# Optimization experiments

Hardware: AMD Instinct MI355X
Metric: run time of the kernel (lower is better)

Reference implementation:

```python
import jax, jax.numpy as jnp
import numpy as np

B, S, H = 1, 2048, 2048
NH = 16            # num attention heads
QLR = 1536         # q_lora_rank
KVLR = 512         # kv_lora_rank
DR = 64            # qk_rope_head_dim
DN = 128           # qk_nope_head_dim
DV = 128           # v_head_dim
DQK = DN + DR      # qk_head_dim = 192
EPS = 1e-6


def rmsnorm(x, w):
    xf = x.astype(jnp.float32)
    var = jnp.mean(xf * xf, axis=-1, keepdims=True)
    return (xf * jax.lax.rsqrt(var + EPS)).astype(x.dtype) * w


def rotate_half(x):
    d = x.shape[-1] // 2
    return jnp.concatenate([-x[..., d:], x[..., :d]], axis=-1)


def rope_interleave(x, cos, sin):
    # x: [b, h, s, d]; de-interleave pairs (even dims -> first half, odd -> second)
    b, h, s, d = x.shape
    x = x.reshape(b, h, s, d // 2, 2).swapaxes(-1, -2).reshape(b, h, s, d)
    return x * cos + rotate_half(x) * sin


def setup_inputs() -> dict:
    key = jax.random.key(0)
    ks = jax.random.split(key, 8)
    std = 0.02
    hidden_states = jax.random.normal(ks[0], (B, S, H), jnp.float32)
    # real rotary cos/sin for a 64-dim rope slice
    pos = jnp.arange(S, dtype=jnp.float32)
    inv_freq = 1.0 / (10000.0 ** (jnp.arange(0, DR, 2, dtype=jnp.float32) / DR))
    ang = pos[:, None] * inv_freq[None, :]            # [S, DR//2]
    emb = jnp.concatenate([ang, ang], axis=-1)        # [S, DR]
    cos = jnp.broadcast_to(jnp.cos(emb)[None], (B, S, DR)).astype(jnp.float32)
    sin = jnp.broadcast_to(jnp.sin(emb)[None], (B, S, DR)).astype(jnp.float32)
    # weights stored [in, out]
    wq_a = jax.random.normal(ks[1], (H, QLR), jnp.float32) * std
    q_ln = jnp.ones((QLR,), jnp.float32)
    wq_b = jax.random.normal(ks[2], (QLR, NH * DQK), jnp.float32) * std
    wkv_a = jax.random.normal(ks[3], (H, KVLR + DR), jnp.float32) * std
    kv_ln = jnp.ones((KVLR,), jnp.float32)
    wkv_b = jax.random.normal(ks[4], (KVLR, NH * (DN + DV)), jnp.float32) * std
    wo = jax.random.normal(ks[5], (NH * DV, H), jnp.float32) * std
    return {"hidden_states": hidden_states, "cos": cos, "sin": sin,
            "wq_a": wq_a, "q_ln": q_ln, "wq_b": wq_b,
            "wkv_a": wkv_a, "kv_ln": kv_ln, "wkv_b": wkv_b, "wo": wo}


def reference(hidden_states, cos, sin, wq_a, q_ln, wq_b, wkv_a, kv_ln, wkv_b, wo):
    b, s, _ = hidden_states.shape
    # low-rank Q: a-proj -> RMSNorm -> b-proj
    q = rmsnorm(hidden_states @ wq_a, q_ln) @ wq_b           # [b, s, NH*DQK]
    q = q.reshape(b, s, NH, DQK).transpose(0, 2, 1, 3)       # [b, NH, s, DQK]
    q_pass, q_rot = q[..., :DN], q[..., DN:]
    # compressed KV with shared rope key
    ckv = hidden_states @ wkv_a                               # [b, s, KVLR+DR]
    kv_c, k_rot = ckv[..., :KVLR], ckv[..., KVLR:]
    kv = (rmsnorm(kv_c, kv_ln) @ wkv_b).reshape(b, s, NH, DN + DV).transpose(0, 2, 1, 3)
    k_pass, v = kv[..., :DN], kv[..., DN:]
    k_rot = k_rot[:, None, :, :]                              # [b, 1, s, DR]
    cos4, sin4 = cos[:, None], sin[:, None]
    q_rot = rope_interleave(q_rot, cos4, sin4)
    k_rot = rope_interleave(k_rot, cos4, sin4)
    k_rot = jnp.broadcast_to(k_rot, (b, NH, s, DR))
    qs = jnp.concatenate([q_pass, q_rot], axis=-1)            # [b, NH, s, DQK]
    ks_ = jnp.concatenate([k_pass, k_rot], axis=-1)
    scaling = DQK ** -0.5
    scores = jnp.einsum('bhqd,bhkd->bhqk', qs, ks_) * scaling
    causal = jnp.tril(jnp.ones((s, s), bool))
    scores = jnp.where(causal, scores, jnp.finfo(scores.dtype).min)
    probs = jax.nn.softmax(scores.astype(jnp.float32), axis=-1).astype(qs.dtype)
    out = jnp.einsum('bhqk,bhkd->bhqd', probs, v)             # [b, NH, s, DV]
    out = out.transpose(0, 2, 1, 3).reshape(b, s, NH * DV)
    return out @ wo
```

## Files before the change

kernel.cpp:

```cpp
#include <hip/hip_runtime.h>
#include <hip/hip_bf16.h>
#include <stdint.h>

#define S_    2048
#define H_    2048
#define NH_   16
#define QLR_  1536
#define KVLR_ 512
#define DR_   64
#define DN_   128
#define DV_   128
#define DQK_  192
#define QW_   (NH_*DQK_)
#define KVW_  (NH_*(DN_+DV_))
#define CKVW_ (KVLR_+DR_)

typedef __attribute__((ext_vector_type(8))) short short8;
typedef __attribute__((ext_vector_type(4))) float floatx4;

__device__ __forceinline__ unsigned short f2bf(float f) {
    unsigned u = __float_as_uint(f);
    unsigned r = u + 0x7fffu + ((u >> 16) & 1u);
    return (unsigned short)(r >> 16);
}
__device__ __forceinline__ float bf2f(unsigned short h) {
    return __uint_as_float(((unsigned)h) << 16);
}
__device__ __forceinline__ void store_out(float* p, float v) { *p = v; }
__device__ __forceinline__ void store_out(unsigned short* p, float v) { *p = f2bf(v); }

typedef const __attribute__((address_space(1))) unsigned int* gas_ptr;
typedef __attribute__((address_space(3))) unsigned int* las_ptr;
__device__ __forceinline__ void gload16(const void* g, void* l) {
    __builtin_amdgcn_global_load_lds((gas_ptr)g, (las_ptr)l, 16, 0, 0);
}

__device__ __forceinline__ int xcd_swz(int orig, int nwg) {
    int q8 = nwg >> 3, r8 = nwg & 7;
    int xcd = orig & 7, jj = orig >> 3;
    return (xcd < r8 ? xcd * (q8 + 1) : r8 * (q8 + 1) + (xcd - r8) * q8) + jj;
}

#define GEMM_STAGE(b, k0) do {                                               \
        _Pragma("unroll")                                                    \
        for (int sub = 0; sub < 2; ++sub) {                                  \
            int m = tid >> 2, k8 = tid & 3;                                  \
            gload16(A + (size_t)(bm + m) * lda + (k0) + sub * 32 + k8 * 8,   \
                    &As[b][sub][tid * 8]);                                   \
        }                                                                    \
        _Pragma("unroll")                                                    \
        for (int sub = 0; sub < 2; ++sub)                                    \
            _Pragma("unroll")                                                \
            for (int j = 0; j < BN / 64; ++j) {                              \
                int ch = j * 256 + tid;                                      \
                int n = ch >> 2, k8 = ch & 3;                                \
                int nrow = bn + n; if (nrow >= N) nrow = N - 1;              \
                gload16(Bt + (size_t)nrow * K + (k0) + sub * 32 + k8 * 8,    \
                        &Bs[b][sub][ch * 8]);                                \
            }                                                                \
    } while (0)

#define GEMM_COMPUTE_SUB(sub) do {                                           \
        short8 a[2], b[NFR];                                                 \
        _Pragma("unroll")                                                    \
        for (int mi = 0; mi < 2; ++mi)                                       \
            a[mi] = *(const short8*)&As[cur][sub][(wm + mi * 16 + cc) * 32 + g * 8]; \
        _Pragma("unroll")                                                    \
        for (int ni = 0; ni < NFR; ++ni)                                     \
            b[ni] = *(const short8*)&Bs[cur][sub][(wn + ni * 16 + cc) * 32 + g * 8]; \
        __builtin_amdgcn_s_setprio(1);                                       \
        _Pragma("unroll")                                                    \
        for (int mi = 0; mi < 2; ++mi)                                       \
            _Pragma("unroll")                                                \
            for (int ni = 0; ni < NFR; ++ni)                                 \
                acc[mi][ni] = __builtin_amdgcn_mfma_f32_16x16x32_bf16(       \
                    a[mi], b[ni], acc[mi][ni], 0, 0, 0);                     \
        __builtin_amdgcn_s_setprio(0);                                       \
    } while (0)

template <typename OutT, int BN>
__global__ __launch_bounds__(256) void gemm_bf16_db(
    const unsigned short* __restrict__ A, const unsigned short* __restrict__ Bt,
    OutT* __restrict__ C, int M, int N, int K, int lda, int ldc)
{
    constexpr int NFR = BN / 32;
    __shared__ unsigned short As[2][2][64 * 32];
    __shared__ unsigned short Bs[2][2][BN * 32];

    const int tid = threadIdx.x;
    const int l = tid & 63;
    const int g = l >> 4, cc = l & 15;
    const int w = tid >> 6;
    const int wm = (w >> 1) * 32, wn = (w & 1) * (BN / 2);

    const int nwg = gridDim.x * gridDim.y;
    const int wg = xcd_swz(blockIdx.y * gridDim.x + blockIdx.x, nwg);
    const int bm = (wg / gridDim.x) * 64;
    const int bn = (wg % gridDim.x) * BN;

    floatx4 acc[2][NFR];
#pragma unroll
    for (int i = 0; i < 2; i++)
#pragma unroll
        for (int j = 0; j < NFR; j++) acc[i][j] = (floatx4){0.f, 0.f, 0.f, 0.f};

    GEMM_STAGE(0, 0);
    __syncthreads();
    int cur = 0;

    for (int k0 = 0; k0 < K; k0 += 64) {
        if (k0 + 64 < K) GEMM_STAGE(cur ^ 1, k0 + 64);
        GEMM_COMPUTE_SUB(0);
        GEMM_COMPUTE_SUB(1);
        __syncthreads();
        cur ^= 1;
    }

#pragma unroll
    for (int mi = 0; mi < 2; ++mi)
#pragma unroll
        for (int ni = 0; ni < NFR; ++ni)
#pragma unroll
            for (int i = 0; i < 4; ++i) {
                int row = bm + wm + mi * 16 + g * 4 + i;
                int col = bn + wn + ni * 16 + cc;
                if (col < N) store_out(&C[(size_t)row * ldc + col], acc[mi][ni][i]);
            }
}

__global__ __launch_bounds__(256) void gemm_bf16_dual(
    const unsigned short* __restrict__ A, const unsigned short* __restrict__ Bt,
    float* __restrict__ C0, float* __restrict__ C1,
    int M, int N, int K, int lda, int ldc0, int ldc1)
{
    constexpr int BN = 128;
    constexpr int NFR = 4;
    __shared__ unsigned short As[2][2][64 * 32];
    __shared__ unsigned short Bs[2][2][BN * 32];

    const int tid = threadIdx.x;
    const int l = tid & 63;
    const int g = l >> 4, cc = l & 15;
    const int w = tid >> 6;
    const int wm = (w >> 1) * 32, wn = (w & 1) * (BN / 2);

    const int nwg = gridDim.x * gridDim.y;
    const int wg = xcd_swz(blockIdx.y * gridDim.x + blockIdx.x, nwg);
    const int bm = (wg / gridDim.x) * 64;
    const int bn = (wg % gridDim.x) * BN;

    floatx4 acc[2][NFR];
#pragma unroll
    for (int i = 0; i < 2; i++)
#pragma unroll
        for (int j = 0; j < NFR; j++) acc[i][j] = (floatx4){0.f, 0.f, 0.f, 0.f};

    GEMM_STAGE(0, 0);
    __syncthreads();
    int cur = 0;

    for (int k0 = 0; k0 < K; k0 += 64) {
        if (k0 + 64 < K) GEMM_STAGE(cur ^ 1, k0 + 64);
        GEMM_COMPUTE_SUB(0);
        GEMM_COMPUTE_SUB(1);
        __syncthreads();
        cur ^= 1;
    }

#pragma unroll
    for (int mi = 0; mi < 2; ++mi)
#pragma unroll
        for (int ni = 0; ni < NFR; ++ni)
#pragma unroll
            for (int i = 0; i < 4; ++i) {
                int row = bm + wm + mi * 16 + g * 4 + i;
                int col = bn + wn + ni * 16 + cc;
                if (col < QLR_)
                    C0[(size_t)row * ldc0 + col] = acc[mi][ni][i];
                else if (col < N)
                    C1[(size_t)row * ldc1 + (col - QLR_)] = acc[mi][ni][i];
            }
}

__global__ __launch_bounds__(256) void cast_bf16(
    const float* __restrict__ in, unsigned short* __restrict__ out, int n)
{
    int i = (blockIdx.x * 256 + threadIdx.x) * 4;
    if (i >= n) return;
    float4 v = *(const float4*)&in[i];
    ushort4 u;
    u.x = f2bf(v.x); u.y = f2bf(v.y); u.z = f2bf(v.z); u.w = f2bf(v.w);
    *(ushort4*)&out[i] = u;
}

__global__ __launch_bounds__(256) void transpose_cast(
    const float* __restrict__ W, unsigned short* __restrict__ Wt, int K, int N,
    float scl)
{
    __shared__ float t[32][33];
    const int n0 = blockIdx.x * 32, k0 = blockIdx.y * 32;
    const int tx = threadIdx.x & 31, ty4 = (threadIdx.x >> 5) * 4;
#pragma unroll
    for (int j = 0; j < 4; ++j)
        t[ty4 + j][tx] = W[(size_t)(k0 + ty4 + j) * N + n0 + tx];
    __syncthreads();
#pragma unroll
    for (int j = 0; j < 4; ++j)
        Wt[(size_t)(n0 + ty4 + j) * K + k0 + tx] = f2bf(t[tx][ty4 + j] * scl);
}

__global__ __launch_bounds__(256) void rmsnorm_bf16out(
    const float* __restrict__ x, const float* __restrict__ w,
    unsigned short* __restrict__ y, int cols, int xstride)
{
    const float* xr = x + (size_t)blockIdx.x * xstride;
    unsigned short* yr = y + (size_t)blockIdx.x * cols;
    const int tid = threadIdx.x;
    float ss = 0.f;
    for (int c = tid; c < cols; c += 256) { float v = xr[c]; ss += v * v; }
#pragma unroll
    for (int off = 32; off > 0; off >>= 1) ss += __shfl_xor(ss, off);
    __shared__ float red[4];
    if ((tid & 63) == 0) red[tid >> 6] = ss;
    __syncthreads();
    ss = red[0] + red[1] + red[2] + red[3];
    const float inv = rsqrtf(ss / (float)cols + 1e-6f);
    for (int c = tid; c < cols; c += 256) yr[c] = f2bf(xr[c] * inv * w[c]);
}

__global__ void rope_q_bf(unsigned short* __restrict__ q,
                          const float* __restrict__ cs, const float* __restrict__ sn)
{
    int t = blockIdx.x * 256 + threadIdx.x;
    int chunk = t >> 5, j = t & 31;
    int s = chunk >> 4, h = chunk & 15;
    unsigned short* x = q + (size_t)s * QW_ + h * DQK_ + DN_;
    float e = bf2f(x[2 * j]), o = bf2f(x[2 * j + 1]);
    float c = cs[s * DR_ + j], si = sn[s * DR_ + j];
    unsigned short u = f2bf(e * c - o * si);
    unsigned short v = f2bf(o * c + e * si);
    x[j] = u; x[j + 32] = v;
}

__global__ __launch_bounds__(256) void prep_k(
    const unsigned short* __restrict__ kvb, const float* __restrict__ ckv,
    const float* __restrict__ cs, const float* __restrict__ sn,
    unsigned short* __restrict__ kg)
{
    const int s = blockIdx.x, tid = threadIdx.x;
    __shared__ unsigned short rot[64];
    if (tid < 32) {
        int j = tid;
        const float* x = ckv + (size_t)s * CKVW_ + KVLR_;
        float e = x[2 * j], o = x[2 * j + 1];
        float c = cs[s * DR_ + j], si = sn[s * DR_ + j];
        rot[j] = f2bf(e * c - o * si);
        rot[j + 32] = f2bf(o * c + e * si);
    }
    __syncthreads();
    const int sw = s & 7;
    for (int ch = tid; ch < 384; ch += 256) {
        int hh = ch / 24, d8 = ch % 24;
        short8 v;
        if (d8 < 16)
            v = *(const short8*)&kvb[(size_t)s * KVW_ + hh * 256 + d8 * 8];
        else
            v = *(const short8*)&rot[(d8 - 16) * 8];
        int d8s = d8 ^ sw;
        *(short8*)&kg[((size_t)hh * S_ + s) * 192 + d8s * 8] = v;
    }
}

__global__ __launch_bounds__(256) void transpose_v(
    const unsigned short* __restrict__ kvb, unsigned short* __restrict__ vt)
{
    __shared__ unsigned short t[32][36];
    const int dv0 = blockIdx.x * 32, s0 = blockIdx.y * 32, h = blockIdx.z;
    const int r = threadIdx.x >> 3, c4 = threadIdx.x & 7;
    ushort4 ld = *(const ushort4*)&kvb[(size_t)(s0 + r) * KVW_ + h * 256 + 128 + dv0 + c4 * 4];
    t[r][c4 * 4 + 0] = ld.x; t[r][c4 * 4 + 1] = ld.y;
    t[r][c4 * 4 + 2] = ld.z; t[r][c4 * 4 + 3] = ld.w;
    __syncthreads();
    ushort4 st;
    st.x = t[c4 * 4 + 0][r]; st.y = t[c4 * 4 + 1][r];
    st.z = t[c4 * 4 + 2][r]; st.w = t[c4 * 4 + 3][r];
    *(ushort4*)&vt[(size_t)(h * 128 + dv0 + r) * S_ + s0 + c4 * 4] = st;
}

__global__ __launch_bounds__(256, 3) void flash_attn7(
    const unsigned short* __restrict__ qg, const unsigned short* __restrict__ kg,
    const unsigned short* __restrict__ vt,
    unsigned short* __restrict__ op0, unsigned short* __restrict__ op1,
    float* __restrict__ mlp)
{
    const int bid = blockIdx.x;
    const int qblk = 31 - (bid >> 5);
    const int low5 = bid & 31;
    const int h = low5 & 15;
    const int sp = low5 >> 4;
    const int pb = h * 32 + qblk;

    __shared__ unsigned short sm[2 * 6144 + 2 * 4096 + 4 * 640];
    unsigned short* Kb = sm;
    unsigned short* Vb = sm + 12288;
    const int tid = threadIdx.x;
    const int w = tid >> 6;
    const int l = tid & 63, g = l >> 4, cc = l & 15;
    unsigned short* Pw = sm + 20480 + w * 640;

    const int qmin = qblk * 64 + w * 16;
    const int q_lane = qmin + cc;
    const int wave_qmax = qmin + 15;
    const int HT = qblk + 1;
    const int kt_begin = sp * HT, kt_end = kt_begin + HT;

    const unsigned short* kh = kg + (size_t)h * S_ * 192;
    const unsigned short* vh = vt + (size_t)(h * 128) * S_;

    short8 qf[6];
    {
        const unsigned short* qb = qg + (size_t)q_lane * QW_ + h * DQK_;
#pragma unroll
        for (int k6 = 0; k6 < 6; ++k6)
            qf[k6] = *(const short8*)&qb[k6 * 32 + g * 8];
    }

    floatx4 accO[8];
#pragma unroll
    for (int nt = 0; nt < 8; ++nt) accO[nt] = (floatx4){0.f, 0.f, 0.f, 0.f};
    float m_r = -1e30f, l_r = 0.f;

#define STAGE_KV(b, kt) do {                                             \
        const unsigned short* ksrc = kh + (size_t)(kt) * 32 * 192;       \
        _Pragma("unroll")                                                \
        for (int j = 0; j < 3; ++j) {                                    \
            int ch = j * 256 + tid;                                      \
            gload16(ksrc + ch * 8, Kb + (b) * 6144 + ch * 8);            \
        }                                                                \
        const int krow = (kt) * 32;                                      \
        _Pragma("unroll")                                                \
        for (int j = 0; j < 2; ++j) {                                    \
            int ch = j * 256 + tid;                                      \
            int dv = ch >> 2, j8 = ch & 3;                               \
            gload16(vh + (size_t)dv * S_ + krow + j8 * 8,                \
                    Vb + (b) * 4096 + ch * 8);                           \
        }                                                                \
    } while (0)

    STAGE_KV(0, kt_begin);
    int cur = 0;

    for (int kt = kt_begin; kt < kt_end; ++kt) {
        const int krow0 = kt * 32;
        __syncthreads();
        if (kt + 1 < kt_end) STAGE_KV(cur ^ 1, kt + 1);

        if (krow0 <= wave_qmax) {
            const unsigned short* Kc = Kb + cur * 6144;
            const unsigned short* Vc = Vb + cur * 4096;
            const int swz = (cc & 7) << 3;

            floatx4 s0 = (floatx4){0.f, 0.f, 0.f, 0.f};
            floatx4 s1 = (floatx4){0.f, 0.f, 0.f, 0.f};
            __builtin_amdgcn_s_setprio(1);
#pragma unroll
            for (int k6 = 0; k6 < 6; ++k6) {
                short8 b0 = *(const short8*)&Kc[cc * 192 + ((k6 * 32 + g * 8) ^ swz)];
                short8 b1 = *(const short8*)&Kc[(16 + cc) * 192 + ((k6 * 32 + g * 8) ^ swz)];
                s0 = __builtin_amdgcn_mfma_f32_16x16x32_bf16(b0, qf[k6], s0, 0, 0, 0);
                s1 = __builtin_amdgcn_mfma_f32_16x16x32_bf16(b1, qf[k6], s1, 0, 0, 0);
            }
            __builtin_amdgcn_s_setprio(0);

            float v0[4], v1[4];
            if (krow0 + 31 <= qmin) {
#pragma unroll
                for (int i = 0; i < 4; ++i) { v0[i] = s0[i]; v1[i] = s1[i]; }
            } else {
#pragma unroll
                for (int i = 0; i < 4; ++i) {
                    v0[i] = (krow0 + g * 4 + i) <= q_lane ? s0[i] : -1e30f;
                    v1[i] = (krow0 + 16 + g * 4 + i) <= q_lane ? s1[i] : -1e30f;
                }
            }
            float mt = fmaxf(fmaxf(fmaxf(v0[0], v0[1]), fmaxf(v0[2], v0[3])),
                             fmaxf(fmaxf(v1[0], v1[1]), fmaxf(v1[2], v1[3])));
            mt = fmaxf(mt, __shfl_xor(mt, 16));
            mt = fmaxf(mt, __shfl_xor(mt, 32));

            if (!__all(mt <= m_r + 6.0f)) {
                float mn = fmaxf(m_r, mt);
                float alpha = exp2f(m_r - mn);
                m_r = mn;
                l_r *= alpha;
                float aB[4];
#pragma unroll
                for (int i = 0; i < 4; ++i) aB[i] = __shfl(alpha, g * 4 + i);
#pragma unroll
                for (int nt = 0; nt < 8; ++nt)
#pragma unroll
                    for (int i = 0; i < 4; ++i) accO[nt][i] *= aB[i];
            }

            float p0[4], p1[4], ps = 0.f;
#pragma unroll
            for (int i = 0; i < 4; ++i) {
                p0[i] = exp2f(v0[i] - m_r);
                p1[i] = exp2f(v1[i] - m_r);
                ps += p0[i] + p1[i];
            }
            ps += __shfl_xor(ps, 16);
            ps += __shfl_xor(ps, 32);
            l_r += ps;

            {
                unsigned pk00, pk01, pk10, pk11;
                asm("v_cvt_pk_bf16_f32 %0, %1, %2" : "=v"(pk00) : "v"(p0[0]), "v"(p0[1]));
                asm("v_cvt_pk_bf16_f32 %0, %1, %2" : "=v"(pk01) : "v"(p0[2]), "v"(p0[3]));
                asm("v_cvt_pk_bf16_f32 %0, %1, %2" : "=v"(pk10) : "v"(p1[0]), "v"(p1[1]));
                asm("v_cvt_pk_bf16_f32 %0, %1, %2" : "=v"(pk11) : "v"(p1[2]), "v"(p1[3]));
                uint2 w0, w1;
                w0.x = pk00; w0.y = pk01;
                w1.x = pk10; w1.y = pk11;
                *(uint2*)&Pw[cc * 40 + g * 4] = w0;
                *(uint2*)&Pw[cc * 40 + 16 + g * 4] = w1;
            }

            short8 pf = *(const short8*)&Pw[cc * 40 + g * 8];
            __builtin_amdgcn_s_setprio(1);
#pragma unroll
            for (int nt = 0; nt < 8; ++nt) {
                short8 vr = *(const short8*)&Vc[(nt * 16 + cc) * 32 + g * 8];
                accO[nt] = __builtin_amdgcn_mfma_f32_16x16x32_bf16(pf, vr, accO[nt], 0, 0, 0);
            }
            __builtin_amdgcn_s_setprio(0);
        }
        cur ^= 1;
    }
#undef STAGE_KV

    float mB[4], lB[4];
#pragma unroll
    for (int i = 0; i < 4; ++i) {
        int src = (g << 4) | (g * 4 + i);
        mB[i] = __shfl(m_r, src);
        lB[i] = __shfl(l_r, src);
    }
    unsigned short* op = sp ? op1 : op0;
#pragma unroll
    for (int nt = 0; nt < 8; ++nt)
#pragma unroll
        for (int i = 0; i < 4; ++i)
            op[(size_t)pb * 8192 + (w * 16 + g * 4 + i) * 128 + nt * 16 + cc] =
                f2bf(accO[nt][i]);
    if (cc == 0) {
#pragma unroll
        for (int i = 0; i < 4; ++i) {
            size_t mi = ((size_t)(sp * 512 + pb) * 64 + w * 16 + g * 4 + i) * 2;
            mlp[mi + 0] = mB[i];
            mlp[mi + 1] = lB[i];
        }
    }
}

__global__ __launch_bounds__(256) void merge_attn(
    const unsigned short* __restrict__ op0, const unsigned short* __restrict__ op1,
    const float* __restrict__ mlp, unsigned short* __restrict__ ao)
{
    const int pb = blockIdx.x;
    const int h = pb >> 5, qblk = pb & 31;
    const int tid = threadIdx.x;
    const int row = tid >> 2, c0 = (tid & 3) * 32;

    const size_t mi0 = ((size_t)pb * 64 + row) * 2;
    const size_t mi1 = ((size_t)(512 + pb) * 64 + row) * 2;
    float m0 = mlp[mi0 + 0], l0 = mlp[mi0 + 1];
    float m1 = mlp[mi1 + 0], l1 = mlp[mi1 + 1];
    float mf = fmaxf(m0, m1);
    float e0 = exp2f(m0 - mf), e1 = exp2f(m1 - mf);
    float inv = 1.f / (l0 * e0 + l1 * e1);
    float w0 = e0 * inv, w1 = e1 * inv;

    const size_t pbase = (size_t)pb * 8192 + row * 128 + c0;
    unsigned short* dst = ao + (size_t)(qblk * 64 + row) * (NH_ * DV_) + h * DV_ + c0;
#pragma unroll
    for (int j = 0; j < 4; ++j) {
        short8 a = *(const short8*)&op0[pbase + j * 8];
        short8 b = *(const short8*)&op1[pbase + j * 8];
        short8 o;
#pragma unroll
        for (int k = 0; k < 8; ++k)
            o[k] = (short)f2bf(bf2f((unsigned short)a[k]) * w0 +
                               bf2f((unsigned short)b[k]) * w1);
        *(short8*)&dst[j * 8] = o;
    }
}

extern "C" void kernel_launch(void* const* d_in, const int* in_sizes, int n_in,
                              void* d_out, int out_size, void* d_ws, size_t ws_size,
                              hipStream_t stream)
{
    const float* hs    = (const float*)d_in[0];
    const float* cosp  = (const float*)d_in[1];
    const float* sinp  = (const float*)d_in[2];
    const float* wq_a  = (const float*)d_in[3];
    const float* q_ln  = (const float*)d_in[4];
    const float* wq_b  = (const float*)d_in[5];
    const float* wkv_a = (const float*)d_in[6];
    const float* kv_ln = (const float*)d_in[7];
    const float* wkv_b = (const float*)d_in[8];
    const float* wo    = (const float*)d_in[9];
    float* out = (float*)d_out;

    char* ws = (char*)d_ws;
    float*          qa     = (float*)(ws);
    float*          ckv    = (float*)(ws + 12582912);
    unsigned short* q_bf   = (unsigned short*)(ws + 17301504);
    unsigned short* kvb    = (unsigned short*)(ws + 29884416);
    unsigned short* hs_bf  = (unsigned short*)(ws + 46661632);
    unsigned short* qa_bf  = (unsigned short*)(ws + 55050240);
    unsigned short* ckv_bf = (unsigned short*)(ws + 61341696);
    unsigned short* ao_bf  = (unsigned short*)(ws + 63438848);
    unsigned short* wt     = (unsigned short*)(ws + 71827456);
    unsigned short* kg     = (unsigned short*)qa;
    unsigned short* vtb    = hs_bf;

    unsigned short* op0 = qa_bf;
    unsigned short* op1 = wt;
    float*          mlp = ckv;

    const float qscale = 0.07216878364870322f * 1.4426950408889634f;

    cast_bf16<<<(S_ * H_) / 1024, 256, 0, stream>>>(hs, hs_bf, S_ * H_);

    transpose_cast<<<dim3(QLR_ / 32, H_ / 32), 256, 0, stream>>>(wq_a, wt, H_, QLR_, 1.f);
    transpose_cast<<<dim3(CKVW_ / 32, H_ / 32), 256, 0, stream>>>(
        wkv_a, wt + (size_t)QLR_ * H_, H_, CKVW_, 1.f);
    gemm_bf16_dual<<<dim3((QLR_ + CKVW_ + 127) / 128, S_ / 64), 256, 0, stream>>>(
        hs_bf, wt, qa, ckv, S_, QLR_ + CKVW_, H_, H_, QLR_, CKVW_);
    rmsnorm_bf16out<<<S_, 256, 0, stream>>>(qa, q_ln, qa_bf, QLR_, QLR_);
    rmsnorm_bf16out<<<S_, 256, 0, stream>>>(ckv, kv_ln, ckv_bf, KVLR_, CKVW_);

    transpose_cast<<<dim3(QW_ / 32, QLR_ / 32), 256, 0, stream>>>(wq_b, wt, QLR_, QW_, qscale);
    gemm_bf16_db<unsigned short, 128><<<dim3(QW_ / 128, S_ / 64), 256, 0, stream>>>(
        qa_bf, wt, q_bf, S_, QW_, QLR_, QLR_, QW_);
    rope_q_bf<<<(S_ * NH_ * 32) / 256, 256, 0, stream>>>(q_bf, cosp, sinp);

    transpose_cast<<<dim3(KVW_ / 32, KVLR_ / 32), 256, 0, stream>>>(wkv_b, wt, KVLR_, KVW_, 1.f);
    gemm_bf16_db<unsigned short, 128><<<dim3(KVW_ / 128, S_ / 64), 256, 0, stream>>>(
        ckv_bf, wt, kvb, S_, KVW_, KVLR_, KVLR_, KVW_);

    prep_k<<<S_, 256, 0, stream>>>(kvb, ckv, cosp, sinp, kg);
    transpose_v<<<dim3(4, 64, 16), 256, 0, stream>>>(kvb, vtb);

    flash_attn7<<<1024, 256, 0, stream>>>(q_bf, kg, vtb, op0, op1, mlp);
    merge_attn<<<512, 256, 0, stream>>>(op0, op1, mlp, ao_bf);

    transpose_cast<<<dim3(H_ / 32, H_ / 32), 256, 0, stream>>>(wo, wt, H_, H_, 1.f);
    gemm_bf16_db<float, 128><<<dim3(H_ / 128, S_ / 64), 256, 0, stream>>>(
        ao_bf, wt, out, S_, H_, NH_ * DV_, NH_ * DV_, H_);
}
```

Measured before the change: 220.7 us.

## Merge q_b and kv_b GEMMs into one launch; widen flash blocks to 128 queries

Runs the wq_b and wkv_b projection GEMMs as a single grouped launch, with both weight transposes done up front, so the two independent GEMMs share one grid and fill the GPU together. The flash attention kernel now uses 512-thread blocks covering 128 query rows across 8 waves. Each K/V tile staged in shared memory is therefore reused by twice as many waves, and the grid is halved. The merge kernel is re-indexed to the new partial-output layout. The risks are the larger shared-memory footprint per block, which may lower occupancy, and coarser causal load balancing.

```diff
diff --git a/kernel.cpp b/kernel.cpp
--- a/kernel.cpp
+++ b/kernel.cpp
@@ -182,6 +182,67 @@
             }
 }
 
+__global__ __launch_bounds__(256) void gemm_bf16_pair(
+    const unsigned short* __restrict__ A0, const unsigned short* __restrict__ Bt0,
+    unsigned short* __restrict__ Cp0, int N0, int K0, int lda0, int ldc0, int gx0, int nwg0,
+    const unsigned short* __restrict__ A1, const unsigned short* __restrict__ Bt1,
+    unsigned short* __restrict__ Cp1, int N1, int K1, int lda1, int ldc1, int gx1, int nwg1)
+{
+    constexpr int BN = 128;
+    constexpr int NFR = 4;
+    __shared__ unsigned short As[2][2][64 * 32];
+    __shared__ unsigned short Bs[2][2][BN * 32];
+
+    const int tid = threadIdx.x;
+    const int l = tid & 63;
+    const int g = l >> 4, cc = l & 15;
+    const int w = tid >> 6;
+    const int wm = (w >> 1) * 32, wn = (w & 1) * (BN / 2);
+
+    const int bid = blockIdx.x;
+    const unsigned short *A, *Bt;
+    unsigned short* C;
+    int N, K, lda, ldc, wg, gx;
+    if (bid < nwg0) {
+        wg = xcd_swz(bid, nwg0); gx = gx0;
+        A = A0; Bt = Bt0; C = Cp0; N = N0; K = K0; lda = lda0; ldc = ldc0;
+    } else {
+        wg = xcd_swz(bid - nwg0, nwg1); gx = gx1;
+        A = A1; Bt = Bt1; C = Cp1; N = N1; K = K1; lda = lda1; ldc = ldc1;
+    }
+    const int bm = (wg / gx) * 64;
+    const int bn = (wg % gx) * BN;
+
+    floatx4 acc[2][NFR];
+#pragma unroll
+    for (int i = 0; i < 2; i++)
+#pragma unroll
+        for (int j = 0; j < NFR; j++) acc[i][j] = (floatx4){0.f, 0.f, 0.f, 0.f};
+
+    GEMM_STAGE(0, 0);
+    __syncthreads();
+    int cur = 0;
+
+    for (int k0 = 0; k0 < K; k0 += 64) {
+        if (k0 + 64 < K) GEMM_STAGE(cur ^ 1, k0 + 64);
+        GEMM_COMPUTE_SUB(0);
+        GEMM_COMPUTE_SUB(1);
+        __syncthreads();
+        cur ^= 1;
+    }
+
+#pragma unroll
+    for (int mi = 0; mi < 2; ++mi)
+#pragma unroll
+        for (int ni = 0; ni < NFR; ++ni)
+#pragma unroll
+            for (int i = 0; i < 4; ++i) {
+                int row = bm + wm + mi * 16 + g * 4 + i;
+                int col = bn + wn + ni * 16 + cc;
+                if (col < N) C[(size_t)row * ldc + col] = f2bf(acc[mi][ni][i]);
+            }
+}
+
 __global__ __launch_bounds__(256) void cast_bf16(
     const float* __restrict__ in, unsigned short* __restrict__ out, int n)
 {
@@ -287,20 +348,20 @@
     *(ushort4*)&vt[(size_t)(h * 128 + dv0 + r) * S_ + s0 + c4 * 4] = st;
 }
 
-__global__ __launch_bounds__(256, 3) void flash_attn7(
+__global__ __launch_bounds__(512, 4) void flash_attn9(
     const unsigned short* __restrict__ qg, const unsigned short* __restrict__ kg,
     const unsigned short* __restrict__ vt,
     unsigned short* __restrict__ op0, unsigned short* __restrict__ op1,
     float* __restrict__ mlp)
 {
     const int bid = blockIdx.x;
-    const int qblk = 31 - (bid >> 5);
+    const int j = 15 - (bid >> 5);
     const int low5 = bid & 31;
     const int h = low5 & 15;
     const int sp = low5 >> 4;
-    const int pb = h * 32 + qblk;
-
-    __shared__ unsigned short sm[2 * 6144 + 2 * 4096 + 4 * 640];
+    const int pb = h * 16 + j;
+
+    __shared__ unsigned short sm[2 * 6144 + 2 * 4096 + 8 * 640];
     unsigned short* Kb = sm;
     unsigned short* Vb = sm + 12288;
     const int tid = threadIdx.x;
@@ -308,11 +369,11 @@
     const int l = tid & 63, g = l >> 4, cc = l & 15;
     unsigned short* Pw = sm + 20480 + w * 640;
 
-    const int qmin = qblk * 64 + w * 16;
+    const int qmin = j * 128 + w * 16;
     const int q_lane = qmin + cc;
     const int wave_qmax = qmin + 15;
-    const int HT = qblk + 1;
-    const int kt_begin = sp * HT, kt_end = kt_begin + HT;
+    const int cnt = 2 * (j + 1);
+    const int kt_begin = sp * cnt, kt_end = kt_begin + cnt;
 
     const unsigned short* kh = kg + (size_t)h * S_ * 192;
     const unsigned short* vh = vt + (size_t)(h * 128) * S_;
@@ -332,18 +393,15 @@
 
 #define STAGE_KV(b, kt) do {                                             \
         const unsigned short* ksrc = kh + (size_t)(kt) * 32 * 192;       \
-        _Pragma("unroll")                                                \
-        for (int j = 0; j < 3; ++j) {                                    \
-            int ch = j * 256 + tid;                                      \
-            gload16(ksrc + ch * 8, Kb + (b) * 6144 + ch * 8);            \
-        }                                                                \
+        gload16(ksrc + tid * 8, Kb + (b) * 6144 + tid * 8);              \
+        if (tid < 256)                                                   \
+            gload16(ksrc + (512 + tid) * 8,                              \
+                    Kb + (b) * 6144 + (512 + tid) * 8);                  \
         const int krow = (kt) * 32;                                      \
-        _Pragma("unroll")                                                \
-        for (int j = 0; j < 2; ++j) {                                    \
-            int ch = j * 256 + tid;                                      \
-            int dv = ch >> 2, j8 = ch & 3;                               \
+        {                                                                \
+            int dv = tid >> 2, j8 = tid & 3;                             \
             gload16(vh + (size_t)dv * S_ + krow + j8 * 8,                \
-                    Vb + (b) * 4096 + ch * 8);                           \
+                    Vb + (b) * 4096 + tid * 8);                          \
         }                                                                \
     } while (0)
 
@@ -451,29 +509,31 @@
     for (int nt = 0; nt < 8; ++nt)
 #pragma unroll
         for (int i = 0; i < 4; ++i)
-            op[(size_t)pb * 8192 + (w * 16 + g * 4 + i) * 128 + nt * 16 + cc] =
+            op[(size_t)pb * 16384 + (w * 16 + g * 4 + i) * 128 + nt * 16 + cc] =
                 f2bf(accO[nt][i]);
     if (cc == 0) {
 #pragma unroll
         for (int i = 0; i < 4; ++i) {
-            size_t mi = ((size_t)(sp * 512 + pb) * 64 + w * 16 + g * 4 + i) * 2;
+            size_t mi = ((size_t)(sp * 256 + pb) * 128 + w * 16 + g * 4 + i) * 2;
             mlp[mi + 0] = mB[i];
             mlp[mi + 1] = lB[i];
         }
     }
 }
 
-__global__ __launch_bounds__(256) void merge_attn(
+__global__ __launch_bounds__(256) void merge_attn9(
     const unsigned short* __restrict__ op0, const unsigned short* __restrict__ op1,
     const float* __restrict__ mlp, unsigned short* __restrict__ ao)
 {
-    const int pb = blockIdx.x;
-    const int h = pb >> 5, qblk = pb & 31;
+    const int bid = blockIdx.x;
+    const int pb = bid >> 1;
+    const int rh = (bid & 1) * 64;
+    const int h = pb >> 4, j = pb & 15;
     const int tid = threadIdx.x;
-    const int row = tid >> 2, c0 = (tid & 3) * 32;
-
-    const size_t mi0 = ((size_t)pb * 64 + row) * 2;
-    const size_t mi1 = ((size_t)(512 + pb) * 64 + row) * 2;
+    const int row = rh + (tid >> 2), c0 = (tid & 3) * 32;
+
+    const size_t mi0 = ((size_t)pb * 128 + row) * 2;
+    const size_t mi1 = ((size_t)(256 + pb) * 128 + row) * 2;
     float m0 = mlp[mi0 + 0], l0 = mlp[mi0 + 1];
     float m1 = mlp[mi1 + 0], l1 = mlp[mi1 + 1];
     float mf = fmaxf(m0, m1);
@@ -481,18 +541,18 @@
     float inv = 1.f / (l0 * e0 + l1 * e1);
     float w0 = e0 * inv, w1 = e1 * inv;
 
-    const size_t pbase = (size_t)pb * 8192 + row * 128 + c0;
-    unsigned short* dst = ao + (size_t)(qblk * 64 + row) * (NH_ * DV_) + h * DV_ + c0;
-#pragma unroll
-    for (int j = 0; j < 4; ++j) {
-        short8 a = *(const short8*)&op0[pbase + j * 8];
-        short8 b = *(const short8*)&op1[pbase + j * 8];
+    const size_t pbase = (size_t)pb * 16384 + row * 128 + c0;
+    unsigned short* dst = ao + (size_t)(j * 128 + row) * (NH_ * DV_) + h * DV_ + c0;
+#pragma unroll
+    for (int s = 0; s < 4; ++s) {
+        short8 a = *(const short8*)&op0[pbase + s * 8];
+        short8 b = *(const short8*)&op1[pbase + s * 8];
         short8 o;
 #pragma unroll
         for (int k = 0; k < 8; ++k)
             o[k] = (short)f2bf(bf2f((unsigned short)a[k]) * w0 +
                                bf2f((unsigned short)b[k]) * w1);
-        *(short8*)&dst[j * 8] = o;
+        *(short8*)&dst[s * 8] = o;
     }
 }
 
@@ -524,6 +584,7 @@
     unsigned short* wt     = (unsigned short*)(ws + 71827456);
     unsigned short* kg     = (unsigned short*)qa;
     unsigned short* vtb    = hs_bf;
+    unsigned short* wbt2   = (unsigned short*)qa;
 
     unsigned short* op0 = qa_bf;
     unsigned short* op1 = wt;
@@ -542,19 +603,17 @@
     rmsnorm_bf16out<<<S_, 256, 0, stream>>>(ckv, kv_ln, ckv_bf, KVLR_, CKVW_);
 
     transpose_cast<<<dim3(QW_ / 32, QLR_ / 32), 256, 0, stream>>>(wq_b, wt, QLR_, QW_, qscale);
-    gemm_bf16_db<unsigned short, 128><<<dim3(QW_ / 128, S_ / 64), 256, 0, stream>>>(
-        qa_bf, wt, q_bf, S_, QW_, QLR_, QLR_, QW_);
+    transpose_cast<<<dim3(KVW_ / 32, KVLR_ / 32), 256, 0, stream>>>(wkv_b, wbt2, KVLR_, KVW_, 1.f);
+    gemm_bf16_pair<<<768 + 1024, 256, 0, stream>>>(
+        qa_bf, wt, q_bf, QW_, QLR_, QLR_, QW_, QW_ / 128, 768,
+        ckv_bf, wbt2, kvb, KVW_, KVLR_, KVLR_, KVW_, KVW_ / 128, 1024);
     rope_q_bf<<<(S_ * NH_ * 32) / 256, 256, 0, stream>>>(q_bf, cosp, sinp);
-
-    transpose_cast<<<dim3(KVW_ / 32, KVLR_ / 32), 256, 0, stream>>>(wkv_b, wt, KVLR_, KVW_, 1.f);
-    gemm_bf16_db<unsigned short, 128><<<dim3(KVW_ / 128, S_ / 64), 256, 0, stream>>>(
-        ckv_bf, wt, kvb, S_, KVW_, KVLR_, KVLR_, KVW_);
 
     prep_k<<<S_, 256, 0, stream>>>(kvb, ckv, cosp, sinp, kg);
     transpose_v<<<dim3(4, 64, 16), 256, 0, stream>>>(kvb, vtb);
 
-    flash_attn7<<<1024, 256, 0, stream>>>(q_bf, kg, vtb, op0, op1, mlp);
-    merge_attn<<<512, 256, 0, stream>>>(op0, op1, mlp, ao_bf);
+    flash_attn9<<<512, 512, 0, stream>>>(q_bf, kg, vtb, op0, op1, mlp);
+    merge_attn9<<<512, 256, 0, stream>>>(op0, op1, mlp, ao_bf);
 
     transpose_cast<<<dim3(H_ / 32, H_ / 32), 256, 0, stream>>>(wo, wt, H_, H_, 1.f);
     gemm_bf16_db<float, 128><<<dim3(H_ / 128, S_ / 64), 256, 0, stream>>>(
```

Measured after the change: 218.2 us. No clear change (-1.1%).
